# Performance work log

Measured on AMD Instinct MI355X. Metric: run time of the kernel, lower is better.

## Reference

```python
import jax, jax.numpy as jnp
import numpy as np

B, W, WIN_IN = 8, 2048, 1024
D, NH, DFF, L, KS = 512, 8, 2048, 4, 4
NGENES, G = 20000, 2048


def _ln(x, g, b, eps=1e-5):
    m = jnp.mean(x, -1, keepdims=True)
    v = jnp.var(x, -1, keepdims=True)
    return (x - m) * jax.lax.rsqrt(v + eps) * g + b


def _mha(q_in, kv_in, qkv_w, qkv_b, out_w, out_b, nh):
    d = q_in.shape[-1]
    hd = d // nh
    wq, wk, wv = qkv_w[:d], qkv_w[d:2 * d], qkv_w[2 * d:]
    bq, bk, bv = qkv_b[:d], qkv_b[d:2 * d], qkv_b[2 * d:]
    q = (q_in @ wq.T + bq).reshape(q_in.shape[0], q_in.shape[1], nh, hd)
    k = (kv_in @ wk.T + bk).reshape(kv_in.shape[0], kv_in.shape[1], nh, hd)
    v = (kv_in @ wv.T + bv).reshape(kv_in.shape[0], kv_in.shape[1], nh, hd)
    scores = jnp.einsum('bqhd,bkhd->bhqk', q, k) / jnp.sqrt(jnp.asarray(hd, q.dtype))
    a = jax.nn.softmax(scores, axis=-1)
    o = jnp.einsum('bhqk,bkhd->bqhd', a, v).reshape(q_in.shape[0], q_in.shape[1], d)
    return o @ out_w.T + out_b


def _posenc(S, d, dtype):
    pos = jnp.arange(S, dtype=jnp.float32)[:, None]
    div = jnp.exp(jnp.arange(0, d, 2, dtype=jnp.float32) * (-np.log(10000.0) / d))
    pe = jnp.zeros((S, d), jnp.float32)
    pe = pe.at[:, 0::2].set(jnp.sin(pos * div)).at[:, 1::2].set(jnp.cos(pos * div))
    return pe.astype(dtype)


def setup_inputs():
    key = jax.random.key(0)
    ks_ = jax.random.split(key, 12)

    def n(k, shape, s=0.02):
        return jax.random.normal(k, shape, jnp.float32) * s

    return dict(
        windows=jax.random.normal(ks_[0], (B, W, WIN_IN), jnp.float32),
        gene_ids=jax.random.randint(ks_[1], (G,), 0, NGENES),
        W_window=n(ks_[2], (D, WIN_IN)),
        enc_qkv_w=n(ks_[3], (L, 3 * D, D)),
        enc_qkv_b=jnp.zeros((L, 3 * D), jnp.float32),
        enc_out_w=n(ks_[4], (L, D, D)),
        enc_out_b=jnp.zeros((L, D), jnp.float32),
        enc_ln1_g=jnp.ones((L, D), jnp.float32),
        enc_ln1_b=jnp.zeros((L, D), jnp.float32),
        enc_ln2_g=jnp.ones((L, D), jnp.float32),
        enc_ln2_b=jnp.zeros((L, D), jnp.float32),
        enc_ff1_w=n(ks_[5], (L, DFF, D)),
        enc_ff1_b=jnp.zeros((L, DFF), jnp.float32),
        enc_ff2_w=n(ks_[6], (L, D, DFF)),
        enc_ff2_b=jnp.zeros((L, D), jnp.float32),
        gene_embed=n(ks_[7], (NGENES, D), 1.0),
        ca_qkv_w=n(ks_[8], (3 * D, D)),
        ca_qkv_b=jnp.zeros((3 * D,), jnp.float32),
        ca_out_w=n(ks_[9], (D, D)),
        ca_out_b=jnp.zeros((D,), jnp.float32),
        ro_ln_g=jnp.ones((D,), jnp.float32),
        ro_ln_b=jnp.zeros((D,), jnp.float32),
        ro_w=n(ks_[10], (1, D)),
        ro_b=jnp.zeros((1,), jnp.float32),
    )


def reference(windows, gene_ids, W_window, enc_qkv_w, enc_qkv_b, enc_out_w,
              enc_out_b, enc_ln1_g, enc_ln1_b, enc_ln2_g, enc_ln2_b,
              enc_ff1_w, enc_ff1_b, enc_ff2_w, enc_ff2_b, gene_embed,
              ca_qkv_w, ca_qkv_b, ca_out_w, ca_out_b, ro_ln_g, ro_ln_b,
              ro_w, ro_b):
    # proj_window (Linear, no bias; dropout inactive in eval)
    x = windows @ W_window.T                          # [B, W, D]
    Bn, Wn, _ = x.shape
    # AvgPool1d(kernel=stride=KS) along the window axis
    x = x.reshape(Bn, Wn // KS, KS, D).mean(axis=2)   # [B, S, D]
    S = x.shape[1]
    x = x + _posenc(S, D, x.dtype)[None]
    # pre-LN TransformerEncoder, relu FFN, no final norm
    for i in range(L):
        h = _ln(x, enc_ln1_g[i], enc_ln1_b[i])
        x = x + _mha(h, h, enc_qkv_w[i], enc_qkv_b[i], enc_out_w[i], enc_out_b[i], NH)
        h = _ln(x, enc_ln2_g[i], enc_ln2_b[i])
        x = x + (jax.nn.relu(h @ enc_ff1_w[i].T + enc_ff1_b[i]) @ enc_ff2_w[i].T + enc_ff2_b[i])
    # gene queries -> cross attention over encoded windows
    q = jnp.broadcast_to(gene_embed[gene_ids][None], (Bn, gene_ids.shape[0], D))
    z = _mha(q, x, ca_qkv_w, ca_qkv_b, ca_out_w, ca_out_b, NH)   # [B, G, D]
    pred = (_ln(z, ro_ln_g, ro_ln_b) @ ro_w.T + ro_b)[..., 0]    # [B, G]
    return pred, z
```

## Files before the change

kernel.cpp:

```cpp
#include <hip/hip_runtime.h>
#include <math.h>


typedef __attribute__((ext_vector_type(8))) short short8v;
typedef __attribute__((ext_vector_type(4))) float float4v;
typedef const __attribute__((address_space(1))) void* gas_t;
typedef __attribute__((address_space(3))) void* las_t;

__device__ inline unsigned short f2bf(float f) {
    unsigned int u = __builtin_bit_cast(unsigned int, f);
    return (unsigned short)((u + 0x7fffu + ((u >> 16) & 1u)) >> 16);
}

__device__ inline unsigned cvt_pk_bf16(float lo, float hi) {
    unsigned r;
    asm("v_cvt_pk_bf16_f32 %0, %1, %2" : "=v"(r) : "v"(lo), "v"(hi));
    return r;
}

__global__ __launch_bounds__(256) void cvt_k(const float* __restrict__ src,
                                             unsigned short* __restrict__ dst, int n4)
{
    int i = blockIdx.x * 256 + threadIdx.x;
    if (i >= n4) return;
    float4 v = ((const float4*)src)[i];
    ushort4 o;
    o.x = f2bf(v.x); o.y = f2bf(v.y); o.z = f2bf(v.z); o.w = f2bf(v.w);
    ((ushort4*)dst)[i] = o;
}

__global__ __launch_bounds__(256) void pool_windows_k(const float* __restrict__ win,
                                                      unsigned short* __restrict__ pw)
{
    int idx = blockIdx.x * 256 + threadIdx.x;
    int n = idx >> 8, c4 = (idx & 255) << 2;
    const float* base = win + (size_t)n * 4096 + c4;
    float4 a = *(const float4*)(base);
    float4 b2 = *(const float4*)(base + 1024);
    float4 c = *(const float4*)(base + 2048);
    float4 d = *(const float4*)(base + 3072);
    ushort4 r;
    r.x = f2bf((a.x + b2.x + c.x + d.x) * 0.25f);
    r.y = f2bf((a.y + b2.y + c.y + d.y) * 0.25f);
    r.z = f2bf((a.z + b2.z + c.z + d.z) * 0.25f);
    r.w = f2bf((a.w + b2.w + c.w + d.w) * 0.25f);
    ((ushort4*)pw)[idx] = r;
}

template<int BM, int BN, bool BIAS, bool BROW, bool RES, bool RELU, bool POSENC, bool O32, bool O16>
__global__ __launch_bounds__(256) void gemm_bf16_k(
    const unsigned short* __restrict__ A, const unsigned short* __restrict__ Bw,
    const float* __restrict__ bias, const float* __restrict__ Res,
    float* __restrict__ C32, unsigned short* __restrict__ C16,
    int M, int N, int K)
{
    constexpr int BK   = (BM == 128) ? 32 : 64;
    constexpr int CPR  = BK / 8;
    constexpr int WR   = (BM == 64 && BN == 128) ? 1 : 2;
    constexpr int WC   = 4 / WR;
    constexpr int MSTEP = BM / WR;
    constexpr int NSTEP = BN / WC;
    constexpr int MFR  = MSTEP / 16;
    constexpr int NFR  = NSTEP / 16;
    constexpr int LPTA = BM * BK / 2048;
    constexpr int LPTB = BN * BK / 2048;
    constexpr int LPT  = LPTA + LPTB;
    __shared__ __align__(16) unsigned short As[2][BM * BK];
    __shared__ __align__(16) unsigned short Bs[2][BN * BK];
    const int tid = threadIdx.x;
    const int lane = tid & 63;
    const int m0 = blockIdx.x * BM, n0 = blockIdx.y * BN;
    const int wid = tid >> 6;
    const int wr = wid / WC, wc = wid % WC;
    const int r = lane & 15, g = lane >> 4;

    const unsigned short* gA[LPTA];
    const unsigned short* gB[LPTB];
    #pragma unroll
    for (int j = 0; j < LPTA; ++j) {
        int c = tid + j * 256, row = c / CPR, cc = c % CPR;
        gA[j] = A + (size_t)(m0 + row) * K + ((cc ^ (row & (CPR - 1))) * 8);
    }
    #pragma unroll
    for (int j = 0; j < LPTB; ++j) {
        int c = tid + j * 256, row = c / CPR, cc = c % CPR;
        gB[j] = Bw + (size_t)(n0 + row) * K + ((cc ^ (row & (CPR - 1))) * 8);
    }

    auto stage = [&](int bi, int k0) {
        #pragma unroll
        for (int j = 0; j < LPTA; ++j)
            __builtin_amdgcn_global_load_lds((gas_t)(gA[j] + k0), (las_t)(&As[bi][(tid + j * 256) * 8]), 16, 0, 0);
        #pragma unroll
        for (int j = 0; j < LPTB; ++j)
            __builtin_amdgcn_global_load_lds((gas_t)(gB[j] + k0), (las_t)(&Bs[bi][(tid + j * 256) * 8]), 16, 0, 0);
    };

    float4v acc[MFR][NFR];
    float4v z4 = {0.f, 0.f, 0.f, 0.f};
    #pragma unroll
    for (int i = 0; i < MFR; ++i)
        #pragma unroll
        for (int j = 0; j < NFR; ++j) acc[i][j] = z4;

    stage(0, 0);
    int buf = 0;
    for (int k0 = 0; k0 < K; k0 += BK) {
        if (k0 + BK < K) {
            stage(buf ^ 1, k0 + BK);
            if constexpr (LPT == 4) asm volatile("s_waitcnt vmcnt(4)" ::: "memory");
            else                    asm volatile("s_waitcnt vmcnt(6)" ::: "memory");
        } else {
            asm volatile("s_waitcnt vmcnt(0)" ::: "memory");
        }
        __builtin_amdgcn_sched_barrier(0);
        __builtin_amdgcn_s_barrier();
        __builtin_amdgcn_sched_barrier(0);
        #pragma unroll
        for (int kk = 0; kk < BK / 32; ++kk) {
            const int cx = ((kk * 4 + g) ^ (r & (CPR - 1))) * 8;
            short8v a[MFR], b[NFR];
            #pragma unroll
            for (int mi = 0; mi < MFR; ++mi)
                a[mi] = *(const short8v*)&As[buf][(MSTEP * wr + 16 * mi + r) * BK + cx];
            #pragma unroll
            for (int ni = 0; ni < NFR; ++ni)
                b[ni] = *(const short8v*)&Bs[buf][(NSTEP * wc + 16 * ni + r) * BK + cx];
            #pragma unroll
            for (int mi = 0; mi < MFR; ++mi)
                #pragma unroll
                for (int ni = 0; ni < NFR; ++ni)
                    acc[mi][ni] = __builtin_amdgcn_mfma_f32_16x16x32_bf16(a[mi], b[ni], acc[mi][ni], 0, 0, 0);
        }
        __builtin_amdgcn_sched_barrier(0);
        __builtin_amdgcn_s_barrier();
        buf ^= 1;
    }

    #pragma unroll
    for (int mi = 0; mi < MFR; ++mi) {
        #pragma unroll
        for (int ni = 0; ni < NFR; ++ni) {
            const int row0 = m0 + MSTEP * wr + 16 * mi + g * 4;
            const int col  = n0 + NSTEP * wc + 16 * ni + r;
            float bv = (BIAS && !BROW) ? bias[col] : 0.f;
            float fr = 0.f;
            if (POSENC) fr = __expf((float)(col & ~1) * -0.01798894600f);
            #pragma unroll
            for (int q = 0; q < 4; ++q) {
                const int row = row0 + q;
                float v = acc[mi][ni][q] + bv;
                if (BIAS && BROW) v += bias[row];
                if (POSENC) {
                    float ang = (float)(row & 511) * fr;
                    v += (col & 1) ? __cosf(ang) : __sinf(ang);
                }
                if (RES) v += Res[(size_t)row * N + col];
                if (RELU) v = fmaxf(v, 0.0f);
                if (O32) C32[(size_t)row * N + col] = v;
                if (O16) C16[(size_t)row * N + col] = f2bf(v);
            }
        }
    }
}

template<bool SPLIT>
__global__ __launch_bounds__(256) void flashc_k(
    const unsigned short* __restrict__ Qp, long long q_bs, int q_rs,
    const unsigned short* __restrict__ Kp, long long k_bs, int k_rs,
    const unsigned short* __restrict__ Vtp, long long v_hs, long long v_bs, int v_rs,
    unsigned short* __restrict__ Op, long long o_bs, int o_rs,
    unsigned short* __restrict__ opart, float2* __restrict__ Ml,
    int nsplit, int nc)
{
    constexpr float C1 = 0.18033688011112042f;
    __shared__ __align__(16) unsigned short Kb[2][64 * 64];
    __shared__ __align__(16) unsigned short Vb[2][64 * 64];
    __shared__ __align__(16) unsigned short Ps[64 * 64];
    const int qt = blockIdx.x, h = blockIdx.y, z = blockIdx.z;
    const int b = z / nsplit, s = z - b * nsplit;
    const unsigned short* Q  = Qp  + (size_t)b * q_bs + (size_t)h * 64;
    const unsigned short* Kg = Kp  + (size_t)b * k_bs + (size_t)h * 64 + (size_t)(s * nc * 64) * k_rs;
    const unsigned short* Vg = Vtp + (size_t)h * v_hs + (size_t)b * v_bs + (size_t)(s * nc) * 64;
    const int q0 = qt * 64;
    const int tid = threadIdx.x, lane = tid & 63, w = tid >> 6;
    const int r = lane & 15, g = lane >> 4;
    const int sw8 = (r & 7) * 8;
    const int cA = (g * 8) ^ sw8;
    const int cB = ((g + 4) * 8) ^ sw8;
    const int prow = (16 * w + r) * 64;

    const unsigned short* qrow = Q + (size_t)(q0 + 16 * w + r) * q_rs + g * 8;
    short8v qf0 = *(const short8v*)(qrow);
    short8v qf1 = *(const short8v*)(qrow + 32);

    const int r0 = tid >> 3, cc = tid & 7;
    const int srcc = (cc ^ (r0 & 7)) * 8;
    auto stage = [&](int bi, int c) {
        const unsigned short* kc_ = Kg + (size_t)c * 64 * k_rs;
        const unsigned short* vc_ = Vg + (size_t)c * 64;
        __builtin_amdgcn_global_load_lds((gas_t)(kc_ + (size_t)r0 * k_rs + srcc),
                                         (las_t)(&Kb[bi][tid * 8]), 16, 0, 0);
        __builtin_amdgcn_global_load_lds((gas_t)(kc_ + (size_t)(r0 + 32) * k_rs + srcc),
                                         (las_t)(&Kb[bi][(tid + 256) * 8]), 16, 0, 0);
        __builtin_amdgcn_global_load_lds((gas_t)(vc_ + (size_t)r0 * v_rs + srcc),
                                         (las_t)(&Vb[bi][tid * 8]), 16, 0, 0);
        __builtin_amdgcn_global_load_lds((gas_t)(vc_ + (size_t)(r0 + 32) * v_rs + srcc),
                                         (las_t)(&Vb[bi][(tid + 256) * 8]), 16, 0, 0);
    };

    float4v acc_o[4];
    float4v z4 = {0.f, 0.f, 0.f, 0.f};
    #pragma unroll
    for (int dt = 0; dt < 4; ++dt) acc_o[dt] = z4;
    float m_own = -INFINITY, l_own = 0.f;

    stage(0, 0);
    __syncthreads();
    int buf = 0;

    for (int c = 0; c < nc; ++c) {
        if (c + 1 < nc) stage(buf ^ 1, c + 1);
        const unsigned short* KL = Kb[buf];
        const unsigned short* VL = Vb[buf];

        __builtin_amdgcn_s_setprio(1);
        float4v accs[4];
        #pragma unroll
        for (int t = 0; t < 4; ++t) {
            accs[t] = z4;
            const unsigned short* krow = KL + (16 * t + r) * 64;
            short8v kf0 = *(const short8v*)(krow + cA);
            short8v kf1 = *(const short8v*)(krow + cB);
            accs[t] = __builtin_amdgcn_mfma_f32_16x16x32_bf16(kf0, qf0, accs[t], 0, 0, 0);
            accs[t] = __builtin_amdgcn_mfma_f32_16x16x32_bf16(kf1, qf1, accs[t], 0, 0, 0);
        }
        __builtin_amdgcn_s_setprio(0);

        float m0_ = fmaxf(fmaxf(accs[0][0], accs[0][1]), fmaxf(accs[0][2], accs[0][3]));
        float m1_ = fmaxf(fmaxf(accs[1][0], accs[1][1]), fmaxf(accs[1][2], accs[1][3]));
        float m2_ = fmaxf(fmaxf(accs[2][0], accs[2][1]), fmaxf(accs[2][2], accs[2][3]));
        float m3_ = fmaxf(fmaxf(accs[3][0], accs[3][1]), fmaxf(accs[3][2], accs[3][3]));
        float sm = fmaxf(fmaxf(m0_, m1_), fmaxf(m2_, m3_));
        sm = fmaxf(sm, __shfl_xor(sm, 16));
        sm = fmaxf(sm, __shfl_xor(sm, 32));

        if (__any(sm > m_own + 64.f)) {
            float mn = fmaxf(m_own, sm);
            float alpha = __builtin_amdgcn_exp2f((m_own - mn) * C1);
            m_own = mn;
            float a0_ = __shfl(alpha, g * 4 + 0);
            float a1_ = __shfl(alpha, g * 4 + 1);
            float a2_ = __shfl(alpha, g * 4 + 2);
            float a3_ = __shfl(alpha, g * 4 + 3);
            #pragma unroll
            for (int dt = 0; dt < 4; ++dt) {
                acc_o[dt][0] *= a0_; acc_o[dt][1] *= a1_;
                acc_o[dt][2] *= a2_; acc_o[dt][3] *= a3_;
            }
            l_own *= alpha;
        }

        const float m2c = m_own * C1;
        float p[4][4];
        float rsum = 0.f;
        #pragma unroll
        for (int t = 0; t < 4; ++t)
            #pragma unroll
            for (int j = 0; j < 4; ++j) {
                float pv = __builtin_amdgcn_exp2f(__builtin_fmaf(accs[t][j], C1, -m2c));
                p[t][j] = pv; rsum += pv;
            }
        rsum += __shfl_xor(rsum, 16);
        rsum += __shfl_xor(rsum, 32);
        l_own += rsum;

        #pragma unroll
        for (int t = 0; t < 4; ++t) {
            uint2 uu;
            uu.x = cvt_pk_bf16(p[t][0], p[t][1]);
            uu.y = cvt_pk_bf16(p[t][2], p[t][3]);
            int pc = (((2 * t + (g >> 1)) * 8) ^ sw8) + (g & 1) * 4;
            *(uint2*)&Ps[prow + pc] = uu;
        }

        __builtin_amdgcn_s_setprio(1);
        short8v pf0 = *(const short8v*)&Ps[prow + cA];
        short8v pf1 = *(const short8v*)&Ps[prow + cB];
        #pragma unroll
        for (int dt = 0; dt < 4; ++dt) {
            const unsigned short* vrow = VL + (16 * dt + r) * 64;
            short8v vf0 = *(const short8v*)(vrow + cA);
            short8v vf1 = *(const short8v*)(vrow + cB);
            acc_o[dt] = __builtin_amdgcn_mfma_f32_16x16x32_bf16(pf0, vf0, acc_o[dt], 0, 0, 0);
            acc_o[dt] = __builtin_amdgcn_mfma_f32_16x16x32_bf16(pf1, vf1, acc_o[dt], 0, 0, 0);
        }
        __builtin_amdgcn_s_setprio(0);

        __syncthreads();
        buf ^= 1;
    }

    float il0 = 1.f / __shfl(l_own, g * 4 + 0);
    float il1 = 1.f / __shfl(l_own, g * 4 + 1);
    float il2 = 1.f / __shfl(l_own, g * 4 + 2);
    float il3 = 1.f / __shfl(l_own, g * 4 + 3);
    if (SPLIT) {
        unsigned short* Ob = opart + ((size_t)(s * 4096 + b * 512)) * 512 + h * 64;
        #pragma unroll
        for (int dt = 0; dt < 4; ++dt) {
            Ob[(size_t)(q0 + 16 * w + g * 4 + 0) * 512 + 16 * dt + r] = f2bf(acc_o[dt][0] * il0);
            Ob[(size_t)(q0 + 16 * w + g * 4 + 1) * 512 + 16 * dt + r] = f2bf(acc_o[dt][1] * il1);
            Ob[(size_t)(q0 + 16 * w + g * 4 + 2) * 512 + 16 * dt + r] = f2bf(acc_o[dt][2] * il2);
            Ob[(size_t)(q0 + 16 * w + g * 4 + 3) * 512 + 16 * dt + r] = f2bf(acc_o[dt][3] * il3);
        }
        if (g == 0)
            Ml[((size_t)(s * 8 + b) * 8 + h) * 512 + q0 + 16 * w + r] = make_float2(m_own, l_own);
    } else {
        unsigned short* O = Op + (size_t)b * o_bs + (size_t)h * 64;
        #pragma unroll
        for (int dt = 0; dt < 4; ++dt) {
            O[(size_t)(q0 + 16 * w + g * 4 + 0) * o_rs + 16 * dt + r] = f2bf(acc_o[dt][0] * il0);
            O[(size_t)(q0 + 16 * w + g * 4 + 1) * o_rs + 16 * dt + r] = f2bf(acc_o[dt][1] * il1);
            O[(size_t)(q0 + 16 * w + g * 4 + 2) * o_rs + 16 * dt + r] = f2bf(acc_o[dt][2] * il2);
            O[(size_t)(q0 + 16 * w + g * 4 + 3) * o_rs + 16 * dt + r] = f2bf(acc_o[dt][3] * il3);
        }
    }
}

template<int NS>
__global__ __launch_bounds__(256) void combine_k(const unsigned short* __restrict__ opart,
                                                 const float2* __restrict__ Ml,
                                                 unsigned short* __restrict__ Oo)
{
    constexpr float C1 = 0.18033688011112042f;
    const int row = blockIdx.x;
    const int b = row >> 9, srow = row & 511;
    const int tid = threadIdx.x;
    const int h = tid >> 5, t = tid & 31;
    float2 ml[NS];
    float m = -INFINITY;
    #pragma unroll
    for (int s = 0; s < NS; ++s) {
        ml[s] = Ml[((size_t)(s * 8 + b) * 8 + h) * 512 + srow];
        m = fmaxf(m, ml[s].x);
    }
    float wgt[NS];
    float wsum = 0.f;
    #pragma unroll
    for (int s = 0; s < NS; ++s) {
        wgt[s] = __builtin_amdgcn_exp2f((ml[s].x - m) * C1) * ml[s].y;
        wsum += wgt[s];
    }
    float inv = 1.f / wsum;
    const int col = h * 64 + t * 2;
    float acc0 = 0.f, acc1 = 0.f;
    #pragma unroll
    for (int s = 0; s < NS; ++s) {
        unsigned u = *(const unsigned*)&opart[((size_t)s * 4096 + row) * 512 + col];
        acc0 += wgt[s] * __builtin_bit_cast(float, (u & 0xffffu) << 16);
        acc1 += wgt[s] * __builtin_bit_cast(float, (u >> 16) << 16);
    }
    *(unsigned*)&Oo[(size_t)row * 512 + col] = cvt_pk_bf16(acc0 * inv, acc1 * inv);
}

__global__ __launch_bounds__(64) void ln_k(const float* __restrict__ X, unsigned short* __restrict__ Y,
                                           const float* __restrict__ g, const float* __restrict__ bt)
{
    int row = blockIdx.x, lane = threadIdx.x;
    const float* x = X + (size_t)row * 512;
    int c0 = lane * 4, c1 = 256 + lane * 4;
    float4 a0 = *(const float4*)&x[c0];
    float4 a1 = *(const float4*)&x[c1];
    float s  = a0.x + a0.y + a0.z + a0.w + a1.x + a1.y + a1.z + a1.w;
    float ss = a0.x * a0.x + a0.y * a0.y + a0.z * a0.z + a0.w * a0.w
             + a1.x * a1.x + a1.y * a1.y + a1.z * a1.z + a1.w * a1.w;
    #pragma unroll
    for (int off = 1; off < 64; off <<= 1) { s += __shfl_xor(s, off); ss += __shfl_xor(ss, off); }
    float mean = s * (1.f / 512.f);
    float var  = ss * (1.f / 512.f) - mean * mean;
    float rs = rsqrtf(var + 1e-5f);
    float4 g0 = *(const float4*)&g[c0], g1 = *(const float4*)&g[c1];
    float4 b0 = *(const float4*)&bt[c0], b1 = *(const float4*)&bt[c1];
    unsigned short* y = Y + (size_t)row * 512;
    ushort4 o0, o1;
    o0.x = f2bf((a0.x - mean) * rs * g0.x + b0.x);  o0.y = f2bf((a0.y - mean) * rs * g0.y + b0.y);
    o0.z = f2bf((a0.z - mean) * rs * g0.z + b0.z);  o0.w = f2bf((a0.w - mean) * rs * g0.w + b0.w);
    o1.x = f2bf((a1.x - mean) * rs * g1.x + b1.x);  o1.y = f2bf((a1.y - mean) * rs * g1.y + b1.y);
    o1.z = f2bf((a1.z - mean) * rs * g1.z + b1.z);  o1.w = f2bf((a1.w - mean) * rs * g1.w + b1.w);
    *(ushort4*)&y[c0] = o0;
    *(ushort4*)&y[c1] = o1;
}

__global__ __launch_bounds__(128) void gather_k(const float* __restrict__ ge, const int* __restrict__ ids,
                                                unsigned short* __restrict__ out)
{
    int gi = blockIdx.x, t = threadIdx.x;
    int id = ids[gi];
    float4 v = *(const float4*)&ge[(size_t)id * 512 + t * 4];
    ushort4 o;
    o.x = f2bf(v.x); o.y = f2bf(v.y); o.z = f2bf(v.z); o.w = f2bf(v.w);
    *(ushort4*)&out[(size_t)gi * 512 + t * 4] = o;
}

__global__ __launch_bounds__(64) void readout_k(const float* __restrict__ Z,
                                                const float* __restrict__ g, const float* __restrict__ bt,
                                                const float* __restrict__ rw, const float* __restrict__ rb,
                                                float* __restrict__ pred)
{
    int row = blockIdx.x, lane = threadIdx.x;
    const float* zr = Z + (size_t)row * 512;
    int c0 = lane * 4, c1 = 256 + lane * 4;
    float4 a0 = *(const float4*)&zr[c0];
    float4 a1 = *(const float4*)&zr[c1];
    float s  = a0.x + a0.y + a0.z + a0.w + a1.x + a1.y + a1.z + a1.w;
    float ss = a0.x * a0.x + a0.y * a0.y + a0.z * a0.z + a0.w * a0.w
             + a1.x * a1.x + a1.y * a1.y + a1.z * a1.z + a1.w * a1.w;
    #pragma unroll
    for (int off = 1; off < 64; off <<= 1) { s += __shfl_xor(s, off); ss += __shfl_xor(ss, off); }
    float mean = s * (1.f / 512.f);
    float var  = ss * (1.f / 512.f) - mean * mean;
    float rs = rsqrtf(var + 1e-5f);
    float4 g0 = *(const float4*)&g[c0], g1 = *(const float4*)&g[c1];
    float4 b0 = *(const float4*)&bt[c0], b1 = *(const float4*)&bt[c1];
    float4 w0 = *(const float4*)&rw[c0], w1 = *(const float4*)&rw[c1];
    float acc = 0.f;
    acc += ((a0.x - mean) * rs * g0.x + b0.x) * w0.x;
    acc += ((a0.y - mean) * rs * g0.y + b0.y) * w0.y;
    acc += ((a0.z - mean) * rs * g0.z + b0.z) * w0.z;
    acc += ((a0.w - mean) * rs * g0.w + b0.w) * w0.w;
    acc += ((a1.x - mean) * rs * g1.x + b1.x) * w1.x;
    acc += ((a1.y - mean) * rs * g1.y + b1.y) * w1.y;
    acc += ((a1.z - mean) * rs * g1.z + b1.z) * w1.z;
    acc += ((a1.w - mean) * rs * g1.w + b1.w) * w1.w;
    #pragma unroll
    for (int off = 1; off < 64; off <<= 1) acc += __shfl_xor(acc, off);
    if (lane == 0) pred[row] = acc + rb[0];
}

extern "C" void kernel_launch(void* const* d_in, const int* in_sizes, int n_in,
                              void* d_out, int out_size, void* d_ws, size_t ws_size,
                              hipStream_t stream)
{
    (void)in_sizes; (void)n_in; (void)out_size; (void)ws_size;
    const float* windows    = (const float*)d_in[0];
    const int*   gene_ids   = (const int*)  d_in[1];
    const float* W_window   = (const float*)d_in[2];
    const float* enc_qkv_w  = (const float*)d_in[3];
    const float* enc_qkv_b  = (const float*)d_in[4];
    const float* enc_out_w  = (const float*)d_in[5];
    const float* enc_out_b  = (const float*)d_in[6];
    const float* enc_ln1_g  = (const float*)d_in[7];
    const float* enc_ln1_b  = (const float*)d_in[8];
    const float* enc_ln2_g  = (const float*)d_in[9];
    const float* enc_ln2_b  = (const float*)d_in[10];
    const float* enc_ff1_w  = (const float*)d_in[11];
    const float* enc_ff1_b  = (const float*)d_in[12];
    const float* enc_ff2_w  = (const float*)d_in[13];
    const float* enc_ff2_b  = (const float*)d_in[14];
    const float* gene_embed = (const float*)d_in[15];
    const float* ca_qkv_w   = (const float*)d_in[16];
    const float* ca_qkv_b   = (const float*)d_in[17];
    const float* ca_out_w   = (const float*)d_in[18];
    const float* ca_out_b   = (const float*)d_in[19];
    const float* ro_ln_g    = (const float*)d_in[20];
    const float* ro_ln_b    = (const float*)d_in[21];
    const float* ro_w       = (const float*)d_in[22];
    const float* ro_b       = (const float*)d_in[23];

    float* pred = (float*)d_out;
    float* z    = pred + (size_t)8 * 2048;

    char* wp = (char*)d_ws;
    float* x = (float*)wp;                       wp += (size_t)4096 * 512 * 4;
    unsigned short* x16   = (unsigned short*)wp; wp += (size_t)4096 * 512 * 2;
    unsigned short* h16   = (unsigned short*)wp; wp += (size_t)4096 * 512 * 2;
    unsigned short* qkv16 = (unsigned short*)wp; wp += (size_t)4096 * 1536 * 2;
    unsigned short* ao16  = (unsigned short*)wp; wp += (size_t)4096 * 512 * 2;
    unsigned short* big16 = (unsigned short*)wp; wp += (size_t)16384 * 512 * 2;
    unsigned short* vt16  = (unsigned short*)wp; wp += (size_t)512 * 4096 * 2;
    unsigned short* wW16     = (unsigned short*)wp; wp += (size_t)512 * 1024 * 2;
    unsigned short* wqkv16   = (unsigned short*)wp; wp += (size_t)4 * 1536 * 512 * 2;
    unsigned short* wout16   = (unsigned short*)wp; wp += (size_t)4 * 512 * 512 * 2;
    unsigned short* wff116   = (unsigned short*)wp; wp += (size_t)4 * 2048 * 512 * 2;
    unsigned short* wff216   = (unsigned short*)wp; wp += (size_t)4 * 512 * 2048 * 2;
    unsigned short* wcaqkv16 = (unsigned short*)wp; wp += (size_t)1536 * 512 * 2;
    unsigned short* wcaout16 = (unsigned short*)wp; wp += (size_t)512 * 512 * 2;
    unsigned short* pw16    = big16;
    unsigned short* ff116   = big16;
    unsigned short* oc16    = big16;
    unsigned short* opart16 = big16;
    float2* mlbuf = (float2*)(qkv16 + (size_t)4096 * 1024);
    unsigned short* ge16  = qkv16;
    unsigned short* qg16  = qkv16 + (size_t)2048 * 512;
    unsigned short* kc16  = qkv16 + (size_t)2 * 2048 * 512;

    auto cvt = [&](const float* s, unsigned short* d, int n) {
        cvt_k<<<(n / 4 + 255) / 256, 256, 0, stream>>>(s, d, n / 4);
    };
    cvt(W_window,  wW16,     512 * 1024);
    cvt(enc_qkv_w, wqkv16,   4 * 1536 * 512);
    cvt(enc_out_w, wout16,   4 * 512 * 512);
    cvt(enc_ff1_w, wff116,   4 * 2048 * 512);
    cvt(enc_ff2_w, wff216,   4 * 512 * 2048);
    cvt(ca_qkv_w,  wcaqkv16, 1536 * 512);
    cvt(ca_out_w,  wcaout16, 512 * 512);

    pool_windows_k<<<4096, 256, 0, stream>>>(windows, pw16);
    gemm_bf16_k<64, 64, false, false, false, false, true, true, false><<<dim3(64, 8), 256, 0, stream>>>(
        pw16, wW16, nullptr, nullptr, x, nullptr, 4096, 512, 1024);

    for (int l = 0; l < 4; ++l) {
        const unsigned short* wl = wqkv16 + (size_t)l * 1536 * 512;
        ln_k<<<4096, 64, 0, stream>>>(x, h16, enc_ln1_g + l * 512, enc_ln1_b + l * 512);
        gemm_bf16_k<64, 64, true, false, false, false, false, false, true><<<dim3(64, 16), 256, 0, stream>>>(
            h16, wl, enc_qkv_b + l * 1536, nullptr, nullptr, qkv16, 4096, 1024, 512);
        gemm_bf16_k<64, 64, true, true, false, false, false, false, true><<<dim3(8, 64), 256, 0, stream>>>(
            wl + (size_t)1024 * 512, h16, enc_qkv_b + l * 1536 + 1024, nullptr,
            nullptr, vt16, 512, 4096, 512);
        flashc_k<true><<<dim3(8, 8, 32), 256, 0, stream>>>(
            qkv16, (long long)512 * 1024, 1024,
            qkv16 + 512, (long long)512 * 1024, 1024,
            vt16, (long long)64 * 4096, 512LL, 4096,
            nullptr, 0LL, 0,
            opart16, mlbuf, 4, 2);
        combine_k<4><<<4096, 256, 0, stream>>>(opart16, mlbuf, ao16);
        gemm_bf16_k<64, 64, true, false, true, false, false, true, false><<<dim3(64, 8), 256, 0, stream>>>(
            ao16, wout16 + (size_t)l * 512 * 512, enc_out_b + l * 512, x, x, nullptr, 4096, 512, 512);
        ln_k<<<4096, 64, 0, stream>>>(x, h16, enc_ln2_g + l * 512, enc_ln2_b + l * 512);
        gemm_bf16_k<64, 64, true, false, false, true, false, false, true><<<dim3(64, 32), 256, 0, stream>>>(
            h16, wff116 + (size_t)l * 2048 * 512, enc_ff1_b + l * 2048, nullptr,
            nullptr, ff116, 4096, 2048, 512);
        if (l == 3)
            gemm_bf16_k<64, 64, true, false, true, false, false, true, true><<<dim3(64, 8), 256, 0, stream>>>(
                ff116, wff216 + (size_t)l * 512 * 2048, enc_ff2_b + l * 512, x, x, x16, 4096, 512, 2048);
        else
            gemm_bf16_k<64, 64, true, false, true, false, false, true, false><<<dim3(64, 8), 256, 0, stream>>>(
                ff116, wff216 + (size_t)l * 512 * 2048, enc_ff2_b + l * 512, x, x, nullptr, 4096, 512, 2048);
    }

    gather_k<<<2048, 128, 0, stream>>>(gene_embed, gene_ids, ge16);
    gemm_bf16_k<64, 64, true, false, false, false, false, false, true><<<dim3(32, 8), 256, 0, stream>>>(
        ge16, wcaqkv16, ca_qkv_b, nullptr, nullptr, qg16, 2048, 512, 512);
    gemm_bf16_k<64, 64, true, false, false, false, false, false, true><<<dim3(64, 8), 256, 0, stream>>>(
        x16, wcaqkv16 + (size_t)512 * 512, ca_qkv_b + 512, nullptr, nullptr, kc16, 4096, 512, 512);
    gemm_bf16_k<64, 64, true, true, false, false, false, false, true><<<dim3(8, 64), 256, 0, stream>>>(
        wcaqkv16 + (size_t)1024 * 512, x16, ca_qkv_b + 1024, nullptr, nullptr, vt16, 512, 4096, 512);
    flashc_k<false><<<dim3(32, 8, 8), 256, 0, stream>>>(
        qg16, 0LL, 512,
        kc16, (long long)512 * 512, 512,
        vt16, (long long)64 * 4096, 512LL, 4096,
        oc16, (long long)2048 * 512, 512,
        nullptr, nullptr, 1, 8);
    gemm_bf16_k<64, 64, true, false, false, false, false, true, false><<<dim3(256, 8), 256, 0, stream>>>(
        oc16, wcaout16, ca_out_b, nullptr, z, nullptr, 16384, 512, 512);

    readout_k<<<16384, 64, 0, stream>>>(z, ro_ln_g, ro_ln_b, ro_w, ro_b, pred);
}
```

Baseline: 538.7 us.

## Triple-buffer GEMM K-loop and fuse weight conversions into one launch

The bf16 GEMM now uses a three-stage LDS ring buffer with prefetch distance two and a fixed BK of 64 with a 2x2 warp layout, so global-to-LDS loads have more time to land before the MFMAs need them. The seven separate weight-conversion launches are merged into a single kernel that picks its source by index range and writes one contiguous bf16 weight region. The extra buffer raises LDS use per block, which can lower occupancy. The hardcoded vmcnt values assume 4 loads per stage, which holds only for 64x64 tiles, so other tile shapes would wait on the wrong count.

New measurement: 560.0 us. 4.0% more time.

```diff
diff --git a/kernel.cpp b/kernel.cpp
--- a/kernel.cpp
+++ b/kernel.cpp
@@ -18,12 +18,21 @@
     return r;
 }
 
-__global__ __launch_bounds__(256) void cvt_k(const float* __restrict__ src,
-                                             unsigned short* __restrict__ dst, int n4)
-{
+__global__ __launch_bounds__(256) void cvt_all_k(
+    const float* __restrict__ s0, const float* __restrict__ s1, const float* __restrict__ s2,
+    const float* __restrict__ s3, const float* __restrict__ s4, const float* __restrict__ s5,
+    const float* __restrict__ s6, unsigned short* __restrict__ dst)
+{
+    constexpr int c1 = 131072, c2 = 917504, c3 = 1179648, c4 = 2228224, c5 = 3276800, c6 = 3473408;
     int i = blockIdx.x * 256 + threadIdx.x;
-    if (i >= n4) return;
-    float4 v = ((const float4*)src)[i];
+    const float* s = s0; int base = 0;
+    if (i >= c1) { s = s1; base = c1; }
+    if (i >= c2) { s = s2; base = c2; }
+    if (i >= c3) { s = s3; base = c3; }
+    if (i >= c4) { s = s4; base = c4; }
+    if (i >= c5) { s = s5; base = c5; }
+    if (i >= c6) { s = s6; base = c6; }
+    float4 v = ((const float4*)s)[i - base];
     ushort4 o;
     o.x = f2bf(v.x); o.y = f2bf(v.y); o.z = f2bf(v.z); o.w = f2bf(v.w);
     ((ushort4*)dst)[i] = o;
@@ -54,10 +63,9 @@
     float* __restrict__ C32, unsigned short* __restrict__ C16,
     int M, int N, int K)
 {
-    constexpr int BK   = (BM == 128) ? 32 : 64;
+    constexpr int BK   = 64;
     constexpr int CPR  = BK / 8;
-    constexpr int WR   = (BM == 64 && BN == 128) ? 1 : 2;
-    constexpr int WC   = 4 / WR;
+    constexpr int WR   = 2, WC = 2;
     constexpr int MSTEP = BM / WR;
     constexpr int NSTEP = BN / WC;
     constexpr int MFR  = MSTEP / 16;
@@ -65,13 +73,13 @@
     constexpr int LPTA = BM * BK / 2048;
     constexpr int LPTB = BN * BK / 2048;
     constexpr int LPT  = LPTA + LPTB;
-    __shared__ __align__(16) unsigned short As[2][BM * BK];
-    __shared__ __align__(16) unsigned short Bs[2][BN * BK];
+    __shared__ __align__(16) unsigned short As[3][BM * BK];
+    __shared__ __align__(16) unsigned short Bs[3][BN * BK];
     const int tid = threadIdx.x;
     const int lane = tid & 63;
     const int m0 = blockIdx.x * BM, n0 = blockIdx.y * BN;
     const int wid = tid >> 6;
-    const int wr = wid / WC, wc = wid % WC;
+    const int wr = wid >> 1, wc = wid & 1;
     const int r = lane & 15, g = lane >> 4;
 
     const unsigned short* gA[LPTA];
@@ -103,13 +111,16 @@
         #pragma unroll
         for (int j = 0; j < NFR; ++j) acc[i][j] = z4;
 
+    const int S = K / BK;
     stage(0, 0);
-    int buf = 0;
-    for (int k0 = 0; k0 < K; k0 += BK) {
-        if (k0 + BK < K) {
-            stage(buf ^ 1, k0 + BK);
-            if constexpr (LPT == 4) asm volatile("s_waitcnt vmcnt(4)" ::: "memory");
-            else                    asm volatile("s_waitcnt vmcnt(6)" ::: "memory");
+    if (S > 1) stage(1, BK);
+    for (int i = 0; i < S; ++i) {
+        const int bi = i % 3;
+        if (i + 2 < S) {
+            stage((i + 2) % 3, (i + 2) * BK);
+            asm volatile("s_waitcnt vmcnt(8)" ::: "memory");
+        } else if (i + 1 < S) {
+            asm volatile("s_waitcnt vmcnt(4)" ::: "memory");
         } else {
             asm volatile("s_waitcnt vmcnt(0)" ::: "memory");
         }
@@ -122,10 +133,10 @@
             short8v a[MFR], b[NFR];
             #pragma unroll
             for (int mi = 0; mi < MFR; ++mi)
-                a[mi] = *(const short8v*)&As[buf][(MSTEP * wr + 16 * mi + r) * BK + cx];
+                a[mi] = *(const short8v*)&As[bi][(MSTEP * wr + 16 * mi + r) * BK + cx];
             #pragma unroll
             for (int ni = 0; ni < NFR; ++ni)
-                b[ni] = *(const short8v*)&Bs[buf][(NSTEP * wc + 16 * ni + r) * BK + cx];
+                b[ni] = *(const short8v*)&Bs[bi][(NSTEP * wc + 16 * ni + r) * BK + cx];
             #pragma unroll
             for (int mi = 0; mi < MFR; ++mi)
                 #pragma unroll
@@ -134,7 +145,7 @@
         }
         __builtin_amdgcn_sched_barrier(0);
         __builtin_amdgcn_s_barrier();
-        buf ^= 1;
+        __builtin_amdgcn_sched_barrier(0);
     }
 
     #pragma unroll
@@ -479,13 +490,14 @@
     unsigned short* ao16  = (unsigned short*)wp; wp += (size_t)4096 * 512 * 2;
     unsigned short* big16 = (unsigned short*)wp; wp += (size_t)16384 * 512 * 2;
     unsigned short* vt16  = (unsigned short*)wp; wp += (size_t)512 * 4096 * 2;
-    unsigned short* wW16     = (unsigned short*)wp; wp += (size_t)512 * 1024 * 2;
-    unsigned short* wqkv16   = (unsigned short*)wp; wp += (size_t)4 * 1536 * 512 * 2;
-    unsigned short* wout16   = (unsigned short*)wp; wp += (size_t)4 * 512 * 512 * 2;
-    unsigned short* wff116   = (unsigned short*)wp; wp += (size_t)4 * 2048 * 512 * 2;
-    unsigned short* wff216   = (unsigned short*)wp; wp += (size_t)4 * 512 * 2048 * 2;
-    unsigned short* wcaqkv16 = (unsigned short*)wp; wp += (size_t)1536 * 512 * 2;
-    unsigned short* wcaout16 = (unsigned short*)wp; wp += (size_t)512 * 512 * 2;
+    unsigned short* wall16 = (unsigned short*)wp;
+    unsigned short* wW16     = wall16;
+    unsigned short* wqkv16   = wW16     + (size_t)512 * 1024;
+    unsigned short* wout16   = wqkv16   + (size_t)4 * 1536 * 512;
+    unsigned short* wff116   = wout16   + (size_t)4 * 512 * 512;
+    unsigned short* wff216   = wff116   + (size_t)4 * 2048 * 512;
+    unsigned short* wcaqkv16 = wff216   + (size_t)4 * 512 * 2048;
+    unsigned short* wcaout16 = wcaqkv16 + (size_t)1536 * 512;
     unsigned short* pw16    = big16;
     unsigned short* ff116   = big16;
     unsigned short* oc16    = big16;
@@ -495,16 +507,8 @@
     unsigned short* qg16  = qkv16 + (size_t)2048 * 512;
     unsigned short* kc16  = qkv16 + (size_t)2 * 2048 * 512;
 
-    auto cvt = [&](const float* s, unsigned short* d, int n) {
-        cvt_k<<<(n / 4 + 255) / 256, 256, 0, stream>>>(s, d, n / 4);
-    };
-    cvt(W_window,  wW16,     512 * 1024);
-    cvt(enc_qkv_w, wqkv16,   4 * 1536 * 512);
-    cvt(enc_out_w, wout16,   4 * 512 * 512);
-    cvt(enc_ff1_w, wff116,   4 * 2048 * 512);
-    cvt(enc_ff2_w, wff216,   4 * 512 * 2048);
-    cvt(ca_qkv_w,  wcaqkv16, 1536 * 512);
-    cvt(ca_out_w,  wcaout16, 512 * 512);
+    cvt_all_k<<<13824, 256, 0, stream>>>(W_window, enc_qkv_w, enc_out_w, enc_ff1_w,
+                                         enc_ff2_w, ca_qkv_w, ca_out_w, wall16);
 
     pool_windows_k<<<4096, 256, 0, stream>>>(windows, pw16);
     gemm_bf16_k<64, 64, false, false, false, false, true, true, false><<<dim3(64, 8), 256, 0, stream>>>(
```
